# Kernel tuning notes

Measured on AMD Instinct MI355X. Metric: run time of the kernel, lower is better.

The kernel has to match this reference:

```python
import jax, jax.numpy as jnp
import numpy as np

N_NODES = 1000
NODE_DIM = 40
SEQ_LEN = 12
IN_FEAT = 32
HID = 64
LAYERS = 3
GDEP = 2
TOPK = 20
TANH_ALPHA = 3.0
PROP_ALPHA = 0.05
LN_EPS = 1e-5


def setup_inputs() -> dict:
    key = jax.random.key(0)
    ks = jax.random.split(key, 20)
    s = 0.1  # weight init scale
    B = 64
    return {
        "x": jax.random.normal(ks[0], (B, N_NODES, SEQ_LEN, IN_FEAT), jnp.float32),
        # graph constructor params
        "emb1": jax.random.normal(ks[1], (N_NODES, NODE_DIM), jnp.float32) * s,
        "emb2": jax.random.normal(ks[2], (N_NODES, NODE_DIM), jnp.float32) * s,
        "lin1_w": jax.random.normal(ks[3], (NODE_DIM, NODE_DIM), jnp.float32) * s,
        "lin1_b": jnp.zeros((NODE_DIM,), jnp.float32),
        "lin2_w": jax.random.normal(ks[4], (NODE_DIM, NODE_DIM), jnp.float32) * s,
        "lin2_b": jnp.zeros((NODE_DIM,), jnp.float32),
        # LSTM (pytorch gate order i,f,g,o)
        "Wih": jax.random.normal(ks[5], (4 * HID, IN_FEAT), jnp.float32) * s,
        "Whh": jax.random.normal(ks[6], (4 * HID, HID), jnp.float32) * s,
        "bih": jnp.zeros((4 * HID,), jnp.float32),
        "bhh": jnp.zeros((4 * HID,), jnp.float32),
        # per-layer linear 64 -> seq_length
        "lin_w": jax.random.normal(ks[7], (LAYERS, SEQ_LEN, HID), jnp.float32) * s,
        "lin_b": jnp.zeros((LAYERS, SEQ_LEN), jnp.float32),
        # mixprop 1: (gdep+1)*12 -> 32
        "mp1_w": jax.random.normal(ks[8], (LAYERS, 32, (GDEP + 1) * SEQ_LEN), jnp.float32) * s,
        "mp1_b": jnp.zeros((LAYERS, 32), jnp.float32),
        # mixprop 2: (gdep+1)*32 -> node_dim
        "mp2_w": jax.random.normal(ks[9], (LAYERS, NODE_DIM, (GDEP + 1) * 32), jnp.float32) * s,
        "mp2_b": jnp.zeros((LAYERS, NODE_DIM), jnp.float32),
        # layernorm affine over (node_dim, N)
        "gamma": jnp.ones((LAYERS, NODE_DIM, N_NODES), jnp.float32),
        "beta": jnp.zeros((LAYERS, NODE_DIM, N_NODES), jnp.float32),
    }


def _graph_constructor(emb1, emb2, lin1_w, lin1_b, lin2_w, lin2_b):
    m1 = jnp.tanh(TANH_ALPHA * (emb1 @ lin1_w.T + lin1_b))
    m2 = jnp.tanh(TANH_ALPHA * (emb2 @ lin2_w.T + lin2_b))
    a = jax.nn.relu(jnp.tanh(TANH_ALPHA * (m1 @ m2.T - m2 @ m1.T)))
    _, idx = jax.lax.top_k(a, TOPK)  # keep top-k neighbors per row
    mask = jnp.zeros_like(a).at[jnp.arange(a.shape[0])[:, None], idx].set(1.0)
    return a * mask


def _lstm_last(x, Wih, Whh, bih, bhh):
    # x: (B, T, IN_FEAT) -> last hidden state (B, HID)
    B = x.shape[0]
    h0 = jnp.zeros((B, HID), x.dtype)
    c0 = jnp.zeros((B, HID), x.dtype)

    def step(carry, xt):
        h, c = carry
        g = xt @ Wih.T + h @ Whh.T + bih + bhh
        i, f, gg, o = jnp.split(g, 4, axis=-1)
        c = jax.nn.sigmoid(f) * c + jax.nn.sigmoid(i) * jnp.tanh(gg)
        h = jax.nn.sigmoid(o) * jnp.tanh(c)
        return (h, c), None

    (h, _), _ = jax.lax.scan(step, (h0, c0), jnp.swapaxes(x, 0, 1))
    return h


def _mixprop(h, adj_norm, w, b):
    # h: (B, C, N); adj_norm: (N, N) row-normalized (adj + I)
    x0 = h
    outs = [h]
    for _ in range(GDEP):
        h = PROP_ALPHA * x0 + (1.0 - PROP_ALPHA) * jnp.einsum('bcw,vw->bcv', h, adj_norm)
        outs.append(h)
    ho = jnp.concatenate(outs, axis=1)  # (B, C*(GDEP+1), N)
    return jnp.einsum('bcn,oc->bon', ho, w) + b[None, :, None]


def _layernorm(h, gamma, beta):
    # normalize over (C, N) dims
    mu = jnp.mean(h, axis=(1, 2), keepdims=True)
    var = jnp.var(h, axis=(1, 2), keepdims=True)
    return (h - mu) * jax.lax.rsqrt(var + LN_EPS) * gamma[None] + beta[None]


def reference(x, emb1, emb2, lin1_w, lin1_b, lin2_w, lin2_b,
              Wih, Whh, bih, bhh, lin_w, lin_b,
              mp1_w, mp1_b, mp2_w, mp2_b, gamma, beta):
    B, N, T, F = x.shape
    adj = _graph_constructor(emb1, emb2, lin1_w, lin1_b, lin2_w, lin2_b)
    adj = adj + jnp.eye(N, dtype=adj.dtype)
    adj_norm = adj / jnp.sum(adj, axis=1, keepdims=True)

    out = _lstm_last(x.reshape(B * N, T, F), Wih, Whh, bih, bhh)  # (B*N, 64)

    h = None
    for j in range(LAYERS):
        hj = out @ lin_w[j].T + lin_b[j]                # (B*N, 12)
        hj = hj.reshape(B, N, SEQ_LEN).transpose(0, 2, 1)  # (B, 12, N)
        hj = jax.nn.relu(_mixprop(hj, adj_norm, mp1_w[j], mp1_b[j]))
        # dropout is identity in eval mode
        hj = _mixprop(hj, adj_norm, mp2_w[j], mp2_b[j])  # (B, node_dim, N)
        h = _layernorm(hj, gamma[j], beta[j])

    return h.transpose(0, 2, 1).reshape(B, N * NODE_DIM)
```

## Files before the change

kernel.cpp:

```cpp
#include <hip/hip_runtime.h>


typedef unsigned short u16;
typedef __attribute__((ext_vector_type(8))) short bf16x8;
typedef __attribute__((ext_vector_type(4))) float fx4;

#define NB 64
#define NNODE 1000
#define TT 12
#define FF 32
#define HH 64
#define DD 40
#define TOPK_ 20
#define EPR2 22

__device__ __forceinline__ float rcp_f(float x) { return __builtin_amdgcn_rcpf(x); }
__device__ __forceinline__ float tanh_f(float x) {
  return fmaf(-2.0f, rcp_f(__expf(2.0f * x) + 1.0f), 1.0f);
}
__device__ __forceinline__ unsigned int cvt_pk(float lo, float hi) {
  unsigned int r;
  asm("v_cvt_pk_bf16_f32 %0, %1, %2" : "=v"(r) : "v"(lo), "v"(hi));
  return r;
}
__device__ __forceinline__ bf16x8 cvt8(const float* p) {
  union { unsigned int u[4]; bf16x8 v; } r;
  #pragma unroll
  for (int e = 0; e < 4; e++) r.u[e] = cvt_pk(p[2 * e], p[2 * e + 1]);
  return r.v;
}
__device__ __forceinline__ bf16x8 cvt8v(float4 a, float4 b) {
  union { unsigned int u[4]; bf16x8 v; } r;
  r.u[0] = cvt_pk(a.x, a.y); r.u[1] = cvt_pk(a.z, a.w);
  r.u[2] = cvt_pk(b.x, b.y); r.u[3] = cvt_pk(b.z, b.w);
  return r.v;
}

__global__ void k_m1m2(const float* __restrict__ emb1, const float* __restrict__ emb2,
                       const float* __restrict__ w1, const float* __restrict__ b1,
                       const float* __restrict__ w2, const float* __restrict__ b2,
                       float* __restrict__ m1, float* __restrict__ m2,
                       const float* __restrict__ lw, const float* __restrict__ lb,
                       const float* __restrict__ p1w, const float* __restrict__ p1b,
                       const float* __restrict__ p2w, const float* __restrict__ p2b,
                       float* __restrict__ wt) {
  int tid = threadIdx.x;
  if (blockIdx.x == 313) {
    for (int i = tid; i < 768; i += 256) { int k = i / 12, s = i % 12; wt[i] = lw[s * 64 + k]; }
    if (tid < 12) wt[768 + tid] = lb[tid];
    for (int i = tid; i < 1152; i += 256) { int c = i / 32, o = i % 32; wt[784 + i] = p1w[o * 36 + c]; }
    if (tid < 32) wt[1936 + tid] = p1b[tid];
    for (int i = tid; i < 3840; i += 256) { int c = i / 40, o = i % 40; wt[1968 + i] = p2w[o * 96 + c]; }
    if (tid < 40) wt[5808 + tid] = p2b[tid];
    return;
  }
  int id = blockIdx.x * 256 + tid;
  if (id >= 2 * NNODE * DD) return;
  int sel = id / (NNODE * DD);
  int r = id % (NNODE * DD);
  int i = r / DD, o = r % DD;
  const float4* emb = (const float4*)((sel ? emb2 : emb1) + i * DD);
  const float4* w = (const float4*)((sel ? w2 : w1) + o * DD);
  float s = (sel ? b2 : b1)[o];
  #pragma unroll
  for (int k4 = 0; k4 < DD / 4; k4++) {
    float4 a = emb[k4], b = w[k4];
    s = fmaf(a.x, b.x, s); s = fmaf(a.y, b.y, s);
    s = fmaf(a.z, b.z, s); s = fmaf(a.w, b.w, s);
  }
  (sel ? m2 : m1)[r] = tanh_f(3.0f * s);
}

__global__ void k_adj(const float* __restrict__ m1, const float* __restrict__ m2,
                      int2* __restrict__ pae) {
  int v = blockIdx.x, tid = threadIdx.x;
  __shared__ float arow[NNODE];
  __shared__ float m1v[DD], m2v[DD];
  if (tid < DD) { m1v[tid] = m1[v * DD + tid]; m2v[tid] = m2[v * DD + tid]; }
  __syncthreads();
  for (int w = tid; w < NNODE; w += 256) {
    const float4* m2r = (const float4*)(m2 + w * DD);
    const float4* m1r = (const float4*)(m1 + w * DD);
    float d1 = 0.f, d2 = 0.f;
    #pragma unroll
    for (int k4 = 0; k4 < DD / 4; k4++) {
      float4 a = m2r[k4], b = m1r[k4];
      d1 = fmaf(m1v[k4 * 4 + 0], a.x, d1); d1 = fmaf(m1v[k4 * 4 + 1], a.y, d1);
      d1 = fmaf(m1v[k4 * 4 + 2], a.z, d1); d1 = fmaf(m1v[k4 * 4 + 3], a.w, d1);
      d2 = fmaf(m2v[k4 * 4 + 0], b.x, d2); d2 = fmaf(m2v[k4 * 4 + 1], b.y, d2);
      d2 = fmaf(m2v[k4 * 4 + 2], b.z, d2); d2 = fmaf(m2v[k4 * 4 + 3], b.w, d2);
    }
    arow[w] = fmaxf(tanh_f(3.0f * (d1 - d2)), 0.0f);
  }
  __syncthreads();
  if (tid >= 64) return;
  int l = tid;
  float rv[16];
  #pragma unroll
  for (int q = 0; q < 16; q++) {
    int idx = q * 64 + l;
    rv[q] = (idx < NNODE) ? arow[idx] : -2.f;
  }
  float rs = 1.f;
  float myv = 0.f; int myi = 0;
  #pragma unroll
  for (int sel = 0; sel < TOPK_; sel++) {
    float bv = rv[0]; int bi = l;
    #pragma unroll
    for (int q = 1; q < 16; q++) {
      int idx = q * 64 + l;
      if (rv[q] > bv) { bv = rv[q]; bi = idx; }
    }
    #pragma unroll
    for (int off = 1; off < 64; off <<= 1) {
      float ov = __shfl_xor(bv, off); int oi = __shfl_xor(bi, off);
      if (ov > bv || (ov == bv && oi < bi)) { bv = ov; bi = oi; }
    }
    rs += bv;
    if (l == sel + 1) { myv = bv; myi = bi; }
    #pragma unroll
    for (int q = 0; q < 16; q++)
      if (q * 64 + l == bi) rv[q] = -2.f;
  }
  float inv = rcp_f(rs);
  if (l == 0)          pae[v * EPR2] = make_int2(v, __float_as_int(inv));
  else if (l <= TOPK_) pae[v * EPR2 + l] = make_int2(myi, __float_as_int(myv * inv));
  else if (l == 21)    pae[v * EPR2 + 21] = make_int2(v, 0);
}

__global__ __launch_bounds__(256, 2)
void k_lstm(const float* __restrict__ x, const float* __restrict__ Wih,
            const float* __restrict__ Whh, const float* __restrict__ bih,
            const float* __restrict__ bhh, const float* __restrict__ wt,
            float* __restrict__ hj) {
  __shared__ __align__(16) u16 whf[2 * 16 * 64 * 8];
  __shared__ __align__(16) u16 hsh[4][16][64];
  __shared__ float lwsh[12 * 64];
  __shared__ float lbsh[12];
  int tid = threadIdx.x, wave = tid >> 6, lane = tid & 63;
  int arow = lane & 15, kg = lane >> 4;

  for (int cc = tid; cc < 2 * 16 * 64; cc += 256) {
    int l = cc & 63, t16 = cc >> 6, ks = t16 >> 4, nt = t16 & 15;
    int row = (nt >> 2) * 64 + (l & 15) * 4 + (nt & 3);
    *(bf16x8*)&whf[cc * 8] = cvt8(Whh + row * 64 + ks * 32 + (l >> 4) * 8);
  }
  for (int i = tid; i < 768; i += 256) { int s = i >> 6, j = i & 63; lwsh[i] = wt[j * 12 + s]; }
  if (tid < 12) lbsh[tid] = wt[768 + tid];
  __syncthreads();

  bf16x8 wi[16];
  float biasv[16];
  #pragma unroll
  for (int nt = 0; nt < 16; nt++) {
    int row = (nt >> 2) * 64 + arow * 4 + (nt & 3);
    wi[nt] = cvt8(Wih + row * 32 + kg * 8);
    biasv[nt] = bih[row] + bhh[row];
  }

  int seq_base = blockIdx.x * 64 + wave * 16;
  const float* xb = x + (size_t)(seq_base + arow) * (TT * FF) + kg * 8;
  float cst[16];
  #pragma unroll
  for (int q = 0; q < 16; q++) cst[q] = 0.f;

  float4 xf0 = *(const float4*)(xb);
  float4 xf1 = *(const float4*)(xb + 4);

  auto STEP = [&](int t, bool first, float (&hq)[16]) {
    unsigned int zo = 0;
    asm volatile("" : "+v"(zo));
    bf16x8 xa = cvt8v(xf0, xf1);
    if (t < TT - 1) {
      xf0 = *(const float4*)(xb + (t + 1) * FF);
      xf1 = *(const float4*)(xb + (t + 1) * FF + 4);
    }
    fx4 acc[16];
    #pragma unroll
    for (int nt = 0; nt < 16; nt++)
      acc[nt] = (fx4){biasv[nt], biasv[nt], biasv[nt], biasv[nt]};
    #pragma unroll
    for (int nt = 0; nt < 16; nt++)
      acc[nt] = __builtin_amdgcn_mfma_f32_16x16x32_bf16(xa, wi[nt], acc[nt], 0, 0, 0);
    if (!first) {
      asm volatile("" ::: "memory");
      bf16x8 ha0 = *(const bf16x8*)&hsh[wave][arow][kg * 8];
      bf16x8 ha1 = *(const bf16x8*)&hsh[wave][arow][32 + kg * 8];
      asm volatile("" ::: "memory");
      #pragma unroll
      for (int nt = 0; nt < 16; nt++) {
        bf16x8 wb = *(const bf16x8*)&whf[(nt * 64 + lane) * 8 + zo];
        acc[nt] = __builtin_amdgcn_mfma_f32_16x16x32_bf16(ha0, wb, acc[nt], 0, 0, 0);
      }
      #pragma unroll
      for (int nt = 0; nt < 16; nt++) {
        bf16x8 wb = *(const bf16x8*)&whf[((16 + nt) * 64 + lane) * 8 + zo];
        acc[nt] = __builtin_amdgcn_mfma_f32_16x16x32_bf16(ha1, wb, acc[nt], 0, 0, 0);
      }
    }
    #pragma unroll
    for (int i = 0; i < 4; i++) {
      #pragma unroll
      for (int njt = 0; njt < 4; njt++) {
        float iv = acc[njt][i], fv = acc[njt + 4][i];
        float gv = acc[njt + 8][i], ov = acc[njt + 12][i];
        float cpv = cst[i * 4 + njt];
        float ei = __expf(-iv), ef = __expf(-fv);
        float eg = __expf(2.0f * gv), eo = __expf(-ov);
        float A = 1.0f + ef;
        float B = (1.0f + ei) * (eg + 1.0f);
        float c = fmaf(cpv, B, (eg - 1.0f) * A) * rcp_f(A * B);
        cst[i * 4 + njt] = c;
        float ec = __expf(2.0f * c);
        hq[i * 4 + njt] = (ec - 1.0f) * rcp_f((ec + 1.0f) * (1.0f + eo));
      }
    }
  };

  #pragma unroll 1
  for (int t = 0; t < TT - 1; t++) {
    float hq[16];
    STEP(t, t == 0, hq);
    #pragma unroll
    for (int i = 0; i < 4; i++) {
      unsigned int p0 = cvt_pk(hq[i * 4 + 0], hq[i * 4 + 1]);
      unsigned int p1 = cvt_pk(hq[i * 4 + 2], hq[i * 4 + 3]);
      *(uint2*)&hsh[wave][kg * 4 + i][arow * 4] = make_uint2(p0, p1);
    }
  }
  float hq[16];
  STEP(TT - 1, false, hq);

  #pragma unroll
  for (int i = 0; i < 4; i++) {
    float a[12];
    #pragma unroll
    for (int s = 0; s < 12; s++) a[s] = 0.f;
    #pragma unroll
    for (int njt = 0; njt < 4; njt++) {
      float hv = hq[i * 4 + njt];
      #pragma unroll
      for (int s = 0; s < 12; s++)
        a[s] = fmaf(hv, lwsh[s * 64 + arow * 4 + njt], a[s]);
    }
    #pragma unroll
    for (int off = 1; off < 16; off <<= 1) {
      #pragma unroll
      for (int s = 0; s < 12; s++) a[s] += __shfl_xor(a[s], off);
    }
    float outv = a[0];
    #pragma unroll
    for (int s = 1; s < 12; s++) outv = (arow == s) ? a[s] : outv;
    if (arow < 12) {
      int gseq = seq_base + kg * 4 + i;
      int bb = gseq / 1000, nn = gseq - bb * 1000;
      hj[(size_t)(bb * 12 + arow) * NNODE + nn] = outv + lbsh[arow];
    }
  }
}

__global__ void k_prop(const float* __restrict__ hin, const int2* __restrict__ pae,
                       float* __restrict__ ho, int C) {
  int blk = blockIdx.x;
  int b = blk / C, c = blk % C;
  __shared__ float r0[NNODE], r1[NNODE];
  int tid = threadIdx.x;
  const float* src = hin + (size_t)(b * C + c) * NNODE;
  float* dst = ho + (size_t)(b * 3 * C) * NNODE;
  for (int n = tid; n < NNODE; n += 256) {
    float vv = src[n]; r0[n] = vv; dst[(size_t)c * NNODE + n] = vv;
  }
  __syncthreads();
  for (int n = tid; n < NNODE; n += 256) {
    const int4* pa4 = (const int4*)(pae + (size_t)n * EPR2);
    float s = 0.f;
    #pragma unroll
    for (int e = 0; e < EPR2 / 2; e++) {
      int4 p = pa4[e];
      s = fmaf(__int_as_float(p.y), r0[p.x], s);
      s = fmaf(__int_as_float(p.w), r0[p.z], s);
    }
    float h1 = 0.05f * r0[n] + 0.95f * s;
    r1[n] = h1; dst[(size_t)(C + c) * NNODE + n] = h1;
  }
  __syncthreads();
  for (int n = tid; n < NNODE; n += 256) {
    const int4* pa4 = (const int4*)(pae + (size_t)n * EPR2);
    float s = 0.f;
    #pragma unroll
    for (int e = 0; e < EPR2 / 2; e++) {
      int4 p = pa4[e];
      s = fmaf(__int_as_float(p.y), r1[p.x], s);
      s = fmaf(__int_as_float(p.w), r1[p.z], s);
    }
    dst[(size_t)(2 * C + c) * NNODE + n] = 0.05f * r0[n] + 0.95f * s;
  }
}

template <int CIN, int COUT>
__global__ void k_proj(const float* __restrict__ hin, const float* __restrict__ wt,
                       const float* __restrict__ bb, float* __restrict__ out, int relu) {
  int id = blockIdx.x * 256 + threadIdx.x;
  int b = id / NNODE, n = id % NNODE;
  float acc[COUT];
  #pragma unroll
  for (int o = 0; o < COUT; o++) acc[o] = bb[o];
  for (int c = 0; c < CIN; c++) {
    float hv = hin[(size_t)(b * CIN + c) * NNODE + n];
    #pragma unroll
    for (int o = 0; o < COUT; o++) acc[o] = fmaf(hv, wt[c * COUT + o], acc[o]);
  }
  #pragma unroll
  for (int o = 0; o < COUT; o++) {
    float vv = acc[o];
    if (relu) vv = fmaxf(vv, 0.f);
    out[(size_t)(b * COUT + o) * NNODE + n] = vv;
  }
}

__global__ void k_lnstat(const float* __restrict__ hj2, float* __restrict__ stat) {
  int b = blockIdx.x, tid = threadIdx.x, lane = tid & 63, wave = tid >> 6;
  const float4* p = (const float4*)(hj2 + (size_t)b * DD * NNODE);
  float s = 0.f, q = 0.f;
  for (int i = tid; i < DD * NNODE / 4; i += 1024) {
    float4 vv = p[i];
    s += vv.x + vv.y + vv.z + vv.w;
    q = fmaf(vv.x, vv.x, q); q = fmaf(vv.y, vv.y, q);
    q = fmaf(vv.z, vv.z, q); q = fmaf(vv.w, vv.w, q);
  }
  for (int off = 32; off; off >>= 1) { s += __shfl_down(s, off); q += __shfl_down(q, off); }
  __shared__ float ss[16], sq[16];
  if (lane == 0) { ss[wave] = s; sq[wave] = q; }
  __syncthreads();
  if (tid == 0) {
    const float invN = 1.0f / (float)(DD * NNODE);
    float S = 0.f, Q = 0.f;
    for (int t = 0; t < 16; t++) { S += ss[t]; Q += sq[t]; }
    float mu = S * invN;
    float var = Q * invN - mu * mu;
    stat[2 * b] = mu; stat[2 * b + 1] = __builtin_amdgcn_rsqf(var + 1e-5f);
  }
}

__global__ void k_lnapply(const float* __restrict__ hj2, const float* __restrict__ stat,
                          const float* __restrict__ gamma, const float* __restrict__ beta,
                          float* __restrict__ out) {
  int id = blockIdx.x * 256 + threadIdx.x;
  int b = id / NNODE, n = id % NNODE;
  float mu = stat[2 * b], rstd = stat[2 * b + 1];
  size_t obase = (size_t)b * (NNODE * DD) + (size_t)n * DD;
  #pragma unroll
  for (int d0 = 0; d0 < DD / 4; d0++) {
    float tt[4];
    #pragma unroll
    for (int q = 0; q < 4; q++) {
      int d = d0 * 4 + q;
      float h0 = hj2[(size_t)(b * DD + d) * NNODE + n];
      tt[q] = (h0 - mu) * rstd * gamma[d * NNODE + n] + beta[d * NNODE + n];
    }
    *(float4*)(out + obase + d0 * 4) = (float4){tt[0], tt[1], tt[2], tt[3]};
  }
}

#define OFF_M1   0
#define OFF_M2   40000
#define OFF_PAE  80000
#define OFF_HJ   4218000
#define OFF_HO1  4986000
#define OFF_O1   7290000
#define OFF_HO2  124000
#define OFF_HJ2  9338000
#define OFF_STAT 11898000
#define OFF_WT   11898128

extern "C" void kernel_launch(void* const* d_in, const int* in_sizes, int n_in,
                              void* d_out, int out_size, void* d_ws, size_t ws_size,
                              hipStream_t stream) {
  (void)in_sizes; (void)n_in; (void)out_size; (void)ws_size;
  const float* x     = (const float*)d_in[0];
  const float* emb1  = (const float*)d_in[1];
  const float* emb2  = (const float*)d_in[2];
  const float* l1w   = (const float*)d_in[3];
  const float* l1b   = (const float*)d_in[4];
  const float* l2w   = (const float*)d_in[5];
  const float* l2b   = (const float*)d_in[6];
  const float* Wih   = (const float*)d_in[7];
  const float* Whh   = (const float*)d_in[8];
  const float* bih   = (const float*)d_in[9];
  const float* bhh   = (const float*)d_in[10];
  const float* lin_w = (const float*)d_in[11];
  const float* lin_b = (const float*)d_in[12];
  const float* mp1w  = (const float*)d_in[13];
  const float* mp1b  = (const float*)d_in[14];
  const float* mp2w  = (const float*)d_in[15];
  const float* mp2b  = (const float*)d_in[16];
  const float* gamma = (const float*)d_in[17];
  const float* beta  = (const float*)d_in[18];

  float* ws   = (float*)d_ws;
  float* m1   = ws + OFF_M1;
  float* m2   = ws + OFF_M2;
  int2*  pae  = (int2*)(ws + OFF_PAE);
  float* hj   = ws + OFF_HJ;
  float* ho1  = ws + OFF_HO1;
  float* o1   = ws + OFF_O1;
  float* ho2  = ws + OFF_HO2;
  float* hj2  = ws + OFF_HJ2;
  float* stat = ws + OFF_STAT;
  float* wt   = ws + OFF_WT;

  k_m1m2<<<dim3(314), dim3(256), 0, stream>>>(emb1, emb2, l1w, l1b, l2w, l2b, m1, m2,
                                              lin_w + 1536, lin_b + 24, mp1w + 2304,
                                              mp1b + 64, mp2w + 7680, mp2b + 80, wt);
  k_adj<<<dim3(NNODE), dim3(256), 0, stream>>>(m1, m2, pae);
  k_lstm<<<dim3(1000), dim3(256), 0, stream>>>(x, Wih, Whh, bih, bhh, wt, hj);
  k_prop<<<dim3(64 * 12), dim3(256), 0, stream>>>(hj, pae, ho1, 12);
  k_proj<36, 32><<<dim3(250), dim3(256), 0, stream>>>(ho1, wt + 784, wt + 1936, o1, 1);
  k_prop<<<dim3(64 * 32), dim3(256), 0, stream>>>(o1, pae, ho2, 32);
  k_proj<96, 40><<<dim3(250), dim3(256), 0, stream>>>(ho2, wt + 1968, wt + 5808, hj2, 0);
  k_lnstat<<<dim3(NB), dim3(1024), 0, stream>>>(hj2, stat);
  k_lnapply<<<dim3(250), dim3(256), 0, stream>>>(hj2, stat, gamma + 80000, beta + 80000,
                                                 (float*)d_out);
}
```

Baseline: 262.2 us.

## Batch four channels per prop block, drop hop-0 copy, four rows per adj block

The propagation kernel now handles four channels per block. It stores them interleaved in shared memory so each neighbour gather reads one float4 and the edge list is read once per four channels. The hop-0 copy into the concatenated buffer is removed; the projection kernel reads the original input and the two propagated hops from separate buffers. The adjacency kernel computes four rows per block, reusing the loaded m1/m2 neighbour vectors, and runs top-k with one wave per row. Costs are fewer blocks (192 and 512 prop blocks, 250 adj blocks) and higher register use, which may lower parallelism.

```diff
diff --git a/kernel.cpp b/kernel.cpp
--- a/kernel.cpp
+++ b/kernel.cpp
@@ -73,33 +73,46 @@
 
 __global__ void k_adj(const float* __restrict__ m1, const float* __restrict__ m2,
                       int2* __restrict__ pae) {
-  int v = blockIdx.x, tid = threadIdx.x;
-  __shared__ float arow[NNODE];
-  __shared__ float m1v[DD], m2v[DD];
-  if (tid < DD) { m1v[tid] = m1[v * DD + tid]; m2v[tid] = m2[v * DD + tid]; }
+  int v0 = blockIdx.x * 4, tid = threadIdx.x;
+  int lane = tid & 63, wave = tid >> 6;
+  __shared__ float arow4[4][1024];
+  __shared__ float m1v4[4][DD], m2v4[4][DD];
+  for (int i = tid; i < 4 * DD; i += 256) {
+    int r = i / DD, k = i % DD;
+    m1v4[r][k] = m1[(v0 + r) * DD + k];
+    m2v4[r][k] = m2[(v0 + r) * DD + k];
+  }
   __syncthreads();
   for (int w = tid; w < NNODE; w += 256) {
     const float4* m2r = (const float4*)(m2 + w * DD);
     const float4* m1r = (const float4*)(m1 + w * DD);
-    float d1 = 0.f, d2 = 0.f;
-    #pragma unroll
-    for (int k4 = 0; k4 < DD / 4; k4++) {
-      float4 a = m2r[k4], b = m1r[k4];
-      d1 = fmaf(m1v[k4 * 4 + 0], a.x, d1); d1 = fmaf(m1v[k4 * 4 + 1], a.y, d1);
-      d1 = fmaf(m1v[k4 * 4 + 2], a.z, d1); d1 = fmaf(m1v[k4 * 4 + 3], a.w, d1);
-      d2 = fmaf(m2v[k4 * 4 + 0], b.x, d2); d2 = fmaf(m2v[k4 * 4 + 1], b.y, d2);
-      d2 = fmaf(m2v[k4 * 4 + 2], b.z, d2); d2 = fmaf(m2v[k4 * 4 + 3], b.w, d2);
-    }
-    arow[w] = fmaxf(tanh_f(3.0f * (d1 - d2)), 0.0f);
-  }
-  __syncthreads();
-  if (tid >= 64) return;
-  int l = tid;
+    float4 a[10], bb[10];
+    #pragma unroll
+    for (int k4 = 0; k4 < 10; k4++) { a[k4] = m2r[k4]; bb[k4] = m1r[k4]; }
+    #pragma unroll
+    for (int r = 0; r < 4; r++) {
+      float d1 = 0.f, d2 = 0.f;
+      #pragma unroll
+      for (int k4 = 0; k4 < 10; k4++) {
+        d1 = fmaf(m1v4[r][k4 * 4 + 0], a[k4].x, d1);
+        d1 = fmaf(m1v4[r][k4 * 4 + 1], a[k4].y, d1);
+        d1 = fmaf(m1v4[r][k4 * 4 + 2], a[k4].z, d1);
+        d1 = fmaf(m1v4[r][k4 * 4 + 3], a[k4].w, d1);
+        d2 = fmaf(m2v4[r][k4 * 4 + 0], bb[k4].x, d2);
+        d2 = fmaf(m2v4[r][k4 * 4 + 1], bb[k4].y, d2);
+        d2 = fmaf(m2v4[r][k4 * 4 + 2], bb[k4].z, d2);
+        d2 = fmaf(m2v4[r][k4 * 4 + 3], bb[k4].w, d2);
+      }
+      arow4[r][w] = fmaxf(tanh_f(3.0f * (d1 - d2)), 0.0f);
+    }
+  }
+  __syncthreads();
+  int v = v0 + wave, l = lane;
   float rv[16];
   #pragma unroll
   for (int q = 0; q < 16; q++) {
     int idx = q * 64 + l;
-    rv[q] = (idx < NNODE) ? arow[idx] : -2.f;
+    rv[q] = (idx < NNODE) ? arow4[wave][idx] : -2.f;
   }
   float rs = 1.f;
   float myv = 0.f; int myi = 0;
@@ -259,56 +272,94 @@
   }
 }
 
-__global__ void k_prop(const float* __restrict__ hin, const int2* __restrict__ pae,
-                       float* __restrict__ ho, int C) {
-  int blk = blockIdx.x;
-  int b = blk / C, c = blk % C;
-  __shared__ float r0[NNODE], r1[NNODE];
+__global__ void k_prop4(const float* __restrict__ hin, const int2* __restrict__ pae,
+                        float* __restrict__ ho, int C) {
+  int NG = C >> 2;
+  int b = blockIdx.x / NG, g = blockIdx.x % NG;
+  int c0 = g * 4;
+  __shared__ __align__(16) float r0t[NNODE][4];
+  __shared__ __align__(16) float r1t[NNODE][4];
   int tid = threadIdx.x;
-  const float* src = hin + (size_t)(b * C + c) * NNODE;
-  float* dst = ho + (size_t)(b * 3 * C) * NNODE;
+  const float* src = hin + ((size_t)b * C + c0) * NNODE;
+  float* dst = ho + (size_t)b * 2 * C * NNODE;
   for (int n = tid; n < NNODE; n += 256) {
-    float vv = src[n]; r0[n] = vv; dst[(size_t)c * NNODE + n] = vv;
+    float4 v;
+    v.x = src[n];
+    v.y = src[NNODE + n];
+    v.z = src[2 * NNODE + n];
+    v.w = src[3 * NNODE + n];
+    *(float4*)&r0t[n][0] = v;
   }
   __syncthreads();
   for (int n = tid; n < NNODE; n += 256) {
     const int4* pa4 = (const int4*)(pae + (size_t)n * EPR2);
-    float s = 0.f;
+    float4 s = {0.f, 0.f, 0.f, 0.f};
     #pragma unroll
     for (int e = 0; e < EPR2 / 2; e++) {
       int4 p = pa4[e];
-      s = fmaf(__int_as_float(p.y), r0[p.x], s);
-      s = fmaf(__int_as_float(p.w), r0[p.z], s);
-    }
-    float h1 = 0.05f * r0[n] + 0.95f * s;
-    r1[n] = h1; dst[(size_t)(C + c) * NNODE + n] = h1;
+      float av = __int_as_float(p.y);
+      float4 rv = *(const float4*)&r0t[p.x][0];
+      s.x = fmaf(av, rv.x, s.x); s.y = fmaf(av, rv.y, s.y);
+      s.z = fmaf(av, rv.z, s.z); s.w = fmaf(av, rv.w, s.w);
+      float aw = __int_as_float(p.w);
+      float4 rw = *(const float4*)&r0t[p.z][0];
+      s.x = fmaf(aw, rw.x, s.x); s.y = fmaf(aw, rw.y, s.y);
+      s.z = fmaf(aw, rw.z, s.z); s.w = fmaf(aw, rw.w, s.w);
+    }
+    float4 x0 = *(const float4*)&r0t[n][0];
+    float4 h1;
+    h1.x = fmaf(0.95f, s.x, 0.05f * x0.x);
+    h1.y = fmaf(0.95f, s.y, 0.05f * x0.y);
+    h1.z = fmaf(0.95f, s.z, 0.05f * x0.z);
+    h1.w = fmaf(0.95f, s.w, 0.05f * x0.w);
+    *(float4*)&r1t[n][0] = h1;
+    dst[(size_t)(c0 + 0) * NNODE + n] = h1.x;
+    dst[(size_t)(c0 + 1) * NNODE + n] = h1.y;
+    dst[(size_t)(c0 + 2) * NNODE + n] = h1.z;
+    dst[(size_t)(c0 + 3) * NNODE + n] = h1.w;
   }
   __syncthreads();
   for (int n = tid; n < NNODE; n += 256) {
     const int4* pa4 = (const int4*)(pae + (size_t)n * EPR2);
-    float s = 0.f;
+    float4 s = {0.f, 0.f, 0.f, 0.f};
     #pragma unroll
     for (int e = 0; e < EPR2 / 2; e++) {
       int4 p = pa4[e];
-      s = fmaf(__int_as_float(p.y), r1[p.x], s);
-      s = fmaf(__int_as_float(p.w), r1[p.z], s);
-    }
-    dst[(size_t)(2 * C + c) * NNODE + n] = 0.05f * r0[n] + 0.95f * s;
-  }
-}
-
-template <int CIN, int COUT>
-__global__ void k_proj(const float* __restrict__ hin, const float* __restrict__ wt,
-                       const float* __restrict__ bb, float* __restrict__ out, int relu) {
+      float av = __int_as_float(p.y);
+      float4 rv = *(const float4*)&r1t[p.x][0];
+      s.x = fmaf(av, rv.x, s.x); s.y = fmaf(av, rv.y, s.y);
+      s.z = fmaf(av, rv.z, s.z); s.w = fmaf(av, rv.w, s.w);
+      float aw = __int_as_float(p.w);
+      float4 rw = *(const float4*)&r1t[p.z][0];
+      s.x = fmaf(aw, rw.x, s.x); s.y = fmaf(aw, rw.y, s.y);
+      s.z = fmaf(aw, rw.z, s.z); s.w = fmaf(aw, rw.w, s.w);
+    }
+    float4 x0 = *(const float4*)&r0t[n][0];
+    dst[(size_t)(C + c0 + 0) * NNODE + n] = fmaf(0.95f, s.x, 0.05f * x0.x);
+    dst[(size_t)(C + c0 + 1) * NNODE + n] = fmaf(0.95f, s.y, 0.05f * x0.y);
+    dst[(size_t)(C + c0 + 2) * NNODE + n] = fmaf(0.95f, s.z, 0.05f * x0.z);
+    dst[(size_t)(C + c0 + 3) * NNODE + n] = fmaf(0.95f, s.w, 0.05f * x0.w);
+  }
+}
+
+template <int C1, int COUT>
+__global__ void k_proj(const float* __restrict__ src0, const float* __restrict__ src12,
+                       const float* __restrict__ wt, const float* __restrict__ bb,
+                       float* __restrict__ out, int relu) {
   int id = blockIdx.x * 256 + threadIdx.x;
   int b = id / NNODE, n = id % NNODE;
   float acc[COUT];
   #pragma unroll
   for (int o = 0; o < COUT; o++) acc[o] = bb[o];
-  for (int c = 0; c < CIN; c++) {
-    float hv = hin[(size_t)(b * CIN + c) * NNODE + n];
+  for (int c = 0; c < C1; c++) {
+    float hv = src0[(size_t)(b * C1 + c) * NNODE + n];
     #pragma unroll
     for (int o = 0; o < COUT; o++) acc[o] = fmaf(hv, wt[c * COUT + o], acc[o]);
+  }
+  for (int c = 0; c < 2 * C1; c++) {
+    float hv = src12[(size_t)(b * 2 * C1 + c) * NNODE + n];
+    #pragma unroll
+    for (int o = 0; o < COUT; o++) acc[o] = fmaf(hv, wt[(C1 + c) * COUT + o], acc[o]);
   }
   #pragma unroll
   for (int o = 0; o < COUT; o++) {
@@ -365,13 +416,13 @@
 #define OFF_M1   0
 #define OFF_M2   40000
 #define OFF_PAE  80000
-#define OFF_HJ   4218000
-#define OFF_HO1  4986000
-#define OFF_O1   7290000
-#define OFF_HO2  124000
-#define OFF_HJ2  9338000
-#define OFF_STAT 11898000
-#define OFF_WT   11898128
+#define OFF_HJ   124000
+#define OFF_HO1  892000
+#define OFF_O1   2428000
+#define OFF_HO2  4476000
+#define OFF_HJ2  8572000
+#define OFF_STAT 11132000
+#define OFF_WT   11132128
 
 extern "C" void kernel_launch(void* const* d_in, const int* in_sizes, int n_in,
                               void* d_out, int out_size, void* d_ws, size_t ws_size,
@@ -412,12 +463,12 @@
   k_m1m2<<<dim3(314), dim3(256), 0, stream>>>(emb1, emb2, l1w, l1b, l2w, l2b, m1, m2,
                                               lin_w + 1536, lin_b + 24, mp1w + 2304,
                                               mp1b + 64, mp2w + 7680, mp2b + 80, wt);
-  k_adj<<<dim3(NNODE), dim3(256), 0, stream>>>(m1, m2, pae);
+  k_adj<<<dim3(250), dim3(256), 0, stream>>>(m1, m2, pae);
   k_lstm<<<dim3(1000), dim3(256), 0, stream>>>(x, Wih, Whh, bih, bhh, wt, hj);
-  k_prop<<<dim3(64 * 12), dim3(256), 0, stream>>>(hj, pae, ho1, 12);
-  k_proj<36, 32><<<dim3(250), dim3(256), 0, stream>>>(ho1, wt + 784, wt + 1936, o1, 1);
-  k_prop<<<dim3(64 * 32), dim3(256), 0, stream>>>(o1, pae, ho2, 32);
-  k_proj<96, 40><<<dim3(250), dim3(256), 0, stream>>>(ho2, wt + 1968, wt + 5808, hj2, 0);
+  k_prop4<<<dim3(64 * 3), dim3(256), 0, stream>>>(hj, pae, ho1, 12);
+  k_proj<12, 32><<<dim3(250), dim3(256), 0, stream>>>(hj, ho1, wt + 784, wt + 1936, o1, 1);
+  k_prop4<<<dim3(64 * 8), dim3(256), 0, stream>>>(o1, pae, ho2, 32);
+  k_proj<32, 40><<<dim3(250), dim3(256), 0, stream>>>(o1, ho2, wt + 1968, wt + 5808, hj2, 0);
   k_lnstat<<<dim3(NB), dim3(1024), 0, stream>>>(hj2, stat);
   k_lnapply<<<dim3(250), dim3(256), 0, stream>>>(hj2, stat, gamma + 80000, beta + 80000,
                                                  (float*)d_out);
```

New measurement: 249.9 us. -4.7%, faster.
